# Optimization experiments

Measured on AMD Instinct MI355X. Metric: run time of the kernel, lower is better.

## Reference

```python
import jax, jax.numpy as jnp
import numpy as np

# Band partition of the 2049 frequency bins (BSRNN-style: narrow low bands, wide high bands)
_WIDTHS = [25] * 10 + [50] * 12 + [100] * 8 + [399]
_STARTS = np.concatenate([[0], np.cumsum(_WIDTHS)])
SUBBANDS = [(int(_STARTS[i]), int(_STARTS[i + 1])) for i in range(len(_WIDTHS))]
C_IN = 2          # stereo complex input channels
OUT_CH = 128      # band embedding dim
EPS = 1e-5        # GroupNorm eps
TOTAL_CH = sum(2 * C_IN * (e - s) for s, e in SUBBANDS)  # 8196


def setup_inputs() -> dict:
    key = jax.random.key(0)
    k1, k2, k3, k4 = jax.random.split(key, 4)
    B, F, T = 8, 2049, 512
    # x is view_as_real of a complex spectrogram: [B, C, F, T, 2]
    x = jax.random.normal(k1, (B, C_IN, F, T), dtype=jnp.float32)
    x = jnp.stack([x, jax.random.normal(k2, (B, C_IN, F, T), dtype=jnp.float32)], axis=-1)
    gamma = jax.random.uniform(k3, (TOTAL_CH,), dtype=jnp.float32)            # GroupNorm weight (concat over bands)
    beta = jax.random.normal(k4, (TOTAL_CH,), dtype=jnp.float32) * 0.1       # GroupNorm bias
    W = jax.random.normal(jax.random.fold_in(key, 5), (OUT_CH, TOTAL_CH), dtype=jnp.float32) * 0.02  # 1x1 conv weights, concat over bands
    b = jax.random.normal(jax.random.fold_in(key, 6), (len(SUBBANDS), OUT_CH), dtype=jnp.float32) * 0.02
    return {"x": x, "gamma": gamma, "beta": beta, "W": W, "b": b}


def reference(x, gamma, beta, W, b):
    # x: [B, C, F, T, 2] (real view of complex spectrogram)
    B, C, F, T, _ = x.shape
    outs = []
    off = 0
    for i, (s, e) in enumerate(SUBBANDS):
        ch = 2 * C * (e - s)
        # moveaxis(-1, 1): [B, 2, C, w, T] -> reshape [B, 2*C*w, T]
        h = jnp.moveaxis(x[:, :, s:e, :, :], -1, 1).reshape(B, ch, T)
        # GroupNorm(1, ch): normalize over (channel, time) per sample
        mu = jnp.mean(h, axis=(1, 2), keepdims=True)
        var = jnp.var(h, axis=(1, 2), keepdims=True)
        g = gamma[off:off + ch][None, :, None]
        bt = beta[off:off + ch][None, :, None]
        hn = (h - mu) * jax.lax.rsqrt(var + EPS) * g + bt
        # 1x1 Conv1d == per-timestep linear: [out, ch] x [B, ch, T] -> [B, out, T]
        y = jnp.einsum('oc,bct->bot', W[:, off:off + ch], hn) + b[i][None, :, None]
        outs.append(y)
        off += ch
    return jnp.stack(outs, axis=2)  # [B, OUT_CH, n_bands, T]
```

## Files before the change

kernel.cpp:

```cpp
#include <hip/hip_runtime.h>
#include <hip/hip_bf16.h>

typedef __attribute__((ext_vector_type(8))) short short8;
typedef __attribute__((ext_vector_type(4))) float f32x4;

#define NBANDS 31
#define BB 8
#define CCH 2
#define FF 2049
#define TTS 512
#define OUTC 128
#define TCH 8196
#define EPSV 1e-5f
#define NTILES 298

__constant__ int c_wid[NBANDS] = {
    25,25,25,25,25,25,25,25,25,25,
    50,50,50,50,50,50,50,50,50,50,50,50,
    100,100,100,100,100,100,100,100,
    399};
__constant__ int c_start[NBANDS] = {
    0,25,50,75,100,125,150,175,200,225,
    250,300,350,400,450,500,550,600,650,700,750,800,
    850,950,1050,1150,1250,1350,1450,1550,
    1650};
__constant__ int c_gb0[NBANDS + 1] = {
    0,2,4,6,8,10,12,14,16,18,
    20,24,28,32,36,40,44,48,52,56,60,64,
    68,75,82,89,96,103,110,117,
    124,149};
__constant__ int c_kpad[NBANDS] = {
    128,128,128,128,128,128,128,128,128,128,
    256,256,256,256,256,256,256,256,256,256,256,256,
    448,448,448,448,448,448,448,448,
    1600};
__constant__ int c_kbase[NBANDS] = {
    0,16384,32768,49152,65536,81920,98304,114688,131072,147456,
    163840,196608,229376,262144,294912,327680,360448,393216,425984,458752,491520,524288,
    557056,614400,671744,729088,786432,843776,901120,958464,
    1015808};
__constant__ int tb16b[NBANDS] = {
    0,4,8,12,16,20,24,28,32,36,
    40,48,56,64,72,80,88,96,104,112,120,128,
    136,150,164,178,192,206,220,234,
    248};
__constant__ int c_order[NBANDS] = {
    30,22,23,24,25,26,27,28,29,
    10,11,12,13,14,15,16,17,18,19,20,21,
    0,1,2,3,4,5,6,7,8,9};

#define NTRANS 2384
#define NWPREP 248
#define NWP2   992

__device__ inline unsigned short f2bf(float f) {
    __hip_bfloat16 h = __float2bfloat16(f);
    unsigned short u;
    __builtin_memcpy(&u, &h, 2);
    return u;
}

__device__ inline void gload_lds16(const void* g, void* l) {
    __builtin_amdgcn_global_load_lds((const __attribute__((address_space(1))) void*)g,
                                     (__attribute__((address_space(3))) void*)l, 16, 0, 0);
}

__global__ __launch_bounds__(256) void prep(const float* __restrict__ x,
                                            const float* __restrict__ W,
                                            const float* __restrict__ gamma,
                                            const float* __restrict__ beta,
                                            const float* __restrict__ bias,
                                            float* __restrict__ st,
                                            float* __restrict__ wgam,
                                            float* __restrict__ wcb,
                                            unsigned short* __restrict__ wgP,
                                            unsigned short* __restrict__ xb16) {
    __shared__ __align__(16) float ltf[16384];
    __shared__ float s1[256], s2[256];
    const int bid = blockIdx.x;
    const int tid = threadIdx.x;

    if (bid < NTRANS) {
        int g   = bid >> 4;
        int ycc = bid & 15;
        int band = 0;
        while (band + 1 < NBANDS && g >= c_gb0[band + 1]) band++;
        int fb = g - c_gb0[band];
        int b  = ycc >> 1;
        int cc = ycc & 1;
        int w = c_wid[band], s = c_start[band];
        int f0 = fb * 16;
        const float* xcc = x + (size_t)(b * CCH + cc) * FF * 1024;

#pragma unroll
        for (int r = 0; r < 16; ++r) {
            int row = s + min(f0 + r, w - 1);
            gload_lds16(xcc + (size_t)row * 1024 + tid * 4, &ltf[r * 1024 + tid * 4]);
        }
        __syncthreads();

        int taug = tb16b[band] + fb * 2 + cc;
        unsigned short* dst = xb16 + ((size_t)b * NTILES + taug) * 16384;
        float sum = 0.f, sq = 0.f;
#pragma unroll
        for (int it = 0; it < 8; ++it) {
            int idx = it * 256 + tid;
            int tb = idx >> 6, lane = idx & 63;
            int l15 = lane & 15, lg = lane >> 4;
            int t = tb * 16 + l15;
            short8 w8;
#pragma unroll
            for (int rr = 0; rr < 4; ++rr) {
                int floc = 4 * lg + rr;
                float2 v = *(const float2*)&ltf[floc * 1024 + t * 2];
                if (f0 + floc >= w) v = make_float2(0.f, 0.f);
                sum += v.x + v.y;
                sq  += v.x * v.x + v.y * v.y;
                w8[2 * rr]     = (short)f2bf(v.x);
                w8[2 * rr + 1] = (short)f2bf(v.y);
            }
            *(short8*)(dst + (size_t)idx * 8) = w8;
        }

        __syncthreads();
        s1[tid] = sum; s2[tid] = sq;
        __syncthreads();
        for (int st_ = 128; st_ > 0; st_ >>= 1) {
            if (tid < st_) { s1[tid] += s1[tid + st_]; s2[tid] += s2[tid + st_]; }
            __syncthreads();
        }
        if (tid == 0) {
            float* dp = st + (size_t)(g * 16 + ycc) * 2;
            dp[0] = s1[0];
            dp[1] = s2[0];
        }
    } else if (bid < NTRANS + NWPREP) {
        int r = bid - NTRANS;
        int band = r >> 3;
        int off = 4 * c_start[band];
        int ch  = 4 * c_wid[band];
        int o = (r & 7) * 16 + (tid >> 4);
        int lane = tid & 15;
        const float* wrow = W + (size_t)o * TCH + off;
        float sg = 0.f, sb = 0.f;
        for (int c = lane; c < ch; c += 16) {
            float wv = wrow[c];
            sg += wv * gamma[off + c];
            sb += wv * beta[off + c];
        }
        for (int m = 8; m; m >>= 1) {
            sg += __shfl_down(sg, m, 16);
            sb += __shfl_down(sb, m, 16);
        }
        if (lane == 0) {
            wgam[band * OUTC + o] = sg;
            wcb[band * OUTC + o]  = sb + bias[band * OUTC + o];
        }
    } else {
        int r = bid - (NTRANS + NWPREP);
        int band = r % NBANDS;
        int gy   = r / NBANDS;
        int w = c_wid[band];
        int s4 = 4 * c_start[band];
        int Kpad = c_kpad[band];
        int base = c_kbase[band];
        int N = OUTC * Kpad;
        for (int idx = gy * 256 + tid; idx < N; idx += 32 * 256) {
            int o = idx / Kpad;
            int k = idx - o * Kpad;
            int tau = k >> 5, fb = tau >> 1, cc = tau & 1;
            int fo = (k & 31) >> 1, ri = k & 1;
            int f = fb * 16 + fo;
            float val = 0.f;
            if (f < w) {
                int c = s4 + ri * 2 * w + cc * w + f;
                val = W[(size_t)o * TCH + c] * gamma[c];
            }
            int slot = (k >> 3) & 7;
            int pos = (k >> 6) * 8192 + o * 64 + ((slot ^ (o & 7)) * 8) + (k & 7);
            wgP[base + pos] = f2bf(val);
        }
    }
}

__global__ __launch_bounds__(256) void gemm_mfma(const unsigned short* __restrict__ xb16,
                                                 const unsigned short* __restrict__ wgP,
                                                 const float* __restrict__ st,
                                                 const float* __restrict__ wgam,
                                                 const float* __restrict__ wcb,
                                                 float* __restrict__ out) {
    const int band = c_order[blockIdx.y];
    const int b    = blockIdx.x >> 2;
    const int tti  = blockIdx.x & 3;
    const int tt0  = tti * 128;
    const int w    = c_wid[band];
    const int nch  = c_kpad[band] >> 6;
    const unsigned short* wgA = wgP + c_kbase[band];

    __shared__ unsigned short lA[2][8192];

    const int tid  = threadIdx.x;
    const int lane = tid & 63;
    const int wv   = tid >> 6;
    const int l15  = lane & 15;
    const int lg   = lane >> 4;

    const unsigned short* xbT = xb16 +
        (((size_t)b * NTILES + tb16b[band]) * 32 + tti * 8 + wv * 2) * 512 + lane * 8;

    f32x4 acc[8][2] = {};
    short8 bA[4], bB[4];

#define LOADB(c, dst) do {                                                     \
    _Pragma("unroll")                                                          \
    for (int kk = 0; kk < 2; ++kk)                                             \
        _Pragma("unroll")                                                      \
        for (int nf = 0; nf < 2; ++nf)                                         \
            dst[kk * 2 + nf] =                                                 \
                *(const short8*)(xbT + (size_t)((2 * (c) + kk) * 32 + nf) * 512); \
} while (0)

#define STAGE(c, buf) do {                                                     \
    const unsigned short* srcc = wgA + (size_t)(c) * 8192;                     \
    _Pragma("unroll")                                                          \
    for (int q = 0; q < 4; ++q)                                                \
        gload_lds16(srcc + q * 2048 + tid * 8, &lA[buf][q * 2048 + tid * 8]);  \
} while (0)

#define COMPUTE(br, buf) do {                                                  \
    _Pragma("unroll")                                                          \
    for (int kk = 0; kk < 2; ++kk) {                                           \
        short8 af[8];                                                          \
        _Pragma("unroll")                                                      \
        for (int m = 0; m < 8; ++m) {                                          \
            int o = m * 16 + l15;                                              \
            int slot = (lg + 4 * kk) ^ (o & 7);                                \
            af[m] = *(const short8*)&lA[buf][o * 64 + slot * 8];               \
        }                                                                      \
        _Pragma("unroll")                                                      \
        for (int nf = 0; nf < 2; ++nf)                                         \
            _Pragma("unroll")                                                  \
            for (int m = 0; m < 8; ++m)                                        \
                acc[m][nf] = __builtin_amdgcn_mfma_f32_16x16x32_bf16(          \
                    af[m], br[kk * 2 + nf], acc[m][nf], 0, 0, 0);              \
    }                                                                          \
} while (0)

    LOADB(0, bA);
    STAGE(0, 0);
    __syncthreads();
    for (int c = 0; c < nch; c += 2) {
        if (c + 1 < nch) { LOADB(c + 1, bB); STAGE(c + 1, 1); }
        COMPUTE(bA, 0);
        __syncthreads();
        if (c + 1 < nch) {
            if (c + 2 < nch) { LOADB(c + 2, bA); STAGE(c + 2, 0); }
            COMPUTE(bB, 1);
            __syncthreads();
        }
    }
#undef LOADB
#undef STAGE
#undef COMPUTE

    float sum = 0.f, sq = 0.f;
    {
        int g0 = c_gb0[band], g1 = c_gb0[band + 1];
        for (int g = g0; g < g1; ++g) {
            const float* p0 = st + (size_t)(g * 16 + b * 2) * 2;
            sum += p0[0] + p0[2];
            sq  += p0[1] + p0[3];
        }
    }
    const float Nf = (float)(w * 2048);
    const float mu = sum / Nf;
    const float rs = rsqrtf(sq / Nf - mu * mu + EPSV);

#pragma unroll
    for (int m = 0; m < 8; ++m) {
#pragma unroll
        for (int r = 0; r < 4; ++r) {
            int o = m * 16 + lg * 4 + r;
            float wg = wgam[band * OUTC + o];
            float cb = wcb[band * OUTC + o];
            size_t rowoff = (((size_t)b * OUTC + o) * NBANDS + band) * TTS;
#pragma unroll
            for (int nf = 0; nf < 2; ++nf) {
                int t = tt0 + wv * 32 + nf * 16 + l15;
                out[rowoff + t] = rs * (acc[m][nf][r] - mu * wg) + cb;
            }
        }
    }
}

extern "C" void kernel_launch(void* const* d_in, const int* in_sizes, int n_in,
                              void* d_out, int out_size, void* d_ws, size_t ws_size,
                              hipStream_t stream) {
    const float* x     = (const float*)d_in[0];
    const float* gamma = (const float*)d_in[1];
    const float* beta  = (const float*)d_in[2];
    const float* W     = (const float*)d_in[3];
    const float* bias  = (const float*)d_in[4];
    float* out = (float*)d_out;
    float* ws  = (float*)d_ws;

    float* st_part = ws;
    float* wgam    = ws + 5120;
    float* wcb     = ws + 9216;
    unsigned short* wgP  = (unsigned short*)(ws + 13312);
    unsigned short* xb16 = (unsigned short*)(ws + 640000);

    prep<<<NTRANS + NWPREP + NWP2, 256, 0, stream>>>(x, W, gamma, beta, bias,
                                                     st_part, wgam, wcb, wgP, xb16);
    gemm_mfma<<<dim3(32, NBANDS), 256, 0, stream>>>(xb16, wgP, st_part, wgam, wcb, out);
}
```

Measured before the change: 105.5 us.

## Split transpose blocks into four sub-blocks with smaller LDS and shuffle reductions

Each prep transpose block now handles 4 frequency rows instead of 16, so there are four times as many blocks and each uses a quarter of the LDS (16KB instead of 64KB). The goal is higher occupancy and better latency hiding in the memory-bound conversion pass. The tree reduction in shared memory is replaced by a wavefront shuffle reduction plus a 4-way sum. Partial stats become four times as numerous, so the workspace offsets move and the GEMM epilogue loops over more partials.

```diff
diff --git a/kernel.cpp b/kernel.cpp
--- a/kernel.cpp
+++ b/kernel.cpp
@@ -49,7 +49,7 @@
     10,11,12,13,14,15,16,17,18,19,20,21,
     0,1,2,3,4,5,6,7,8,9};
 
-#define NTRANS 2384
+#define NTRANS 9536
 #define NWPREP 248
 #define NWP2   992
 
@@ -75,25 +75,27 @@
                                             float* __restrict__ wcb,
                                             unsigned short* __restrict__ wgP,
                                             unsigned short* __restrict__ xb16) {
-    __shared__ __align__(16) float ltf[16384];
-    __shared__ float s1[256], s2[256];
+    __shared__ __align__(16) float ltf[4096];
+    __shared__ float s1[4], s2[4];
     const int bid = blockIdx.x;
     const int tid = threadIdx.x;
 
     if (bid < NTRANS) {
-        int g   = bid >> 4;
+        int g2  = bid >> 4;
         int ycc = bid & 15;
+        int g   = g2 >> 2;
+        int sub = g2 & 3;
         int band = 0;
         while (band + 1 < NBANDS && g >= c_gb0[band + 1]) band++;
         int fb = g - c_gb0[band];
         int b  = ycc >> 1;
         int cc = ycc & 1;
         int w = c_wid[band], s = c_start[band];
-        int f0 = fb * 16;
+        int f0 = fb * 16 + sub * 4;
         const float* xcc = x + (size_t)(b * CCH + cc) * FF * 1024;
 
 #pragma unroll
-        for (int r = 0; r < 16; ++r) {
+        for (int r = 0; r < 4; ++r) {
             int row = s + min(f0 + r, w - 1);
             gload_lds16(xcc + (size_t)row * 1024 + tid * 4, &ltf[r * 1024 + tid * 4]);
         }
@@ -103,36 +105,34 @@
         unsigned short* dst = xb16 + ((size_t)b * NTILES + taug) * 16384;
         float sum = 0.f, sq = 0.f;
 #pragma unroll
-        for (int it = 0; it < 8; ++it) {
-            int idx = it * 256 + tid;
-            int tb = idx >> 6, lane = idx & 63;
-            int l15 = lane & 15, lg = lane >> 4;
+        for (int i = 0; i < 2; ++i) {
+            int virt = i * 256 + tid;
+            int tb = virt >> 4, l15 = virt & 15;
             int t = tb * 16 + l15;
             short8 w8;
 #pragma unroll
             for (int rr = 0; rr < 4; ++rr) {
-                int floc = 4 * lg + rr;
-                float2 v = *(const float2*)&ltf[floc * 1024 + t * 2];
-                if (f0 + floc >= w) v = make_float2(0.f, 0.f);
+                float2 v = *(const float2*)&ltf[rr * 1024 + t * 2];
+                if (f0 + rr >= w) v = make_float2(0.f, 0.f);
                 sum += v.x + v.y;
                 sq  += v.x * v.x + v.y * v.y;
                 w8[2 * rr]     = (short)f2bf(v.x);
                 w8[2 * rr + 1] = (short)f2bf(v.y);
             }
-            *(short8*)(dst + (size_t)idx * 8) = w8;
-        }
-
+            *(short8*)(dst + ((size_t)tb * 64 + sub * 16 + l15) * 8) = w8;
+        }
+
+        for (int m = 32; m; m >>= 1) {
+            sum += __shfl_down(sum, m);
+            sq  += __shfl_down(sq, m);
+        }
+        int lane = tid & 63, wv = tid >> 6;
+        if (lane == 0) { s1[wv] = sum; s2[wv] = sq; }
         __syncthreads();
-        s1[tid] = sum; s2[tid] = sq;
-        __syncthreads();
-        for (int st_ = 128; st_ > 0; st_ >>= 1) {
-            if (tid < st_) { s1[tid] += s1[tid + st_]; s2[tid] += s2[tid + st_]; }
-            __syncthreads();
-        }
         if (tid == 0) {
-            float* dp = st + (size_t)(g * 16 + ycc) * 2;
-            dp[0] = s1[0];
-            dp[1] = s2[0];
+            float* dp = st + (size_t)(g2 * 16 + ycc) * 2;
+            dp[0] = s1[0] + s1[1] + s1[2] + s1[3];
+            dp[1] = s2[0] + s2[1] + s2[2] + s2[3];
         }
     } else if (bid < NTRANS + NWPREP) {
         int r = bid - NTRANS;
@@ -265,7 +265,7 @@
 
     float sum = 0.f, sq = 0.f;
     {
-        int g0 = c_gb0[band], g1 = c_gb0[band + 1];
+        int g0 = 4 * c_gb0[band], g1 = 4 * c_gb0[band + 1];
         for (int g = g0; g < g1; ++g) {
             const float* p0 = st + (size_t)(g * 16 + b * 2) * 2;
             sum += p0[0] + p0[2];
@@ -305,9 +305,9 @@
     float* ws  = (float*)d_ws;
 
     float* st_part = ws;
-    float* wgam    = ws + 5120;
-    float* wcb     = ws + 9216;
-    unsigned short* wgP  = (unsigned short*)(ws + 13312);
+    float* wgam    = ws + 19456;
+    float* wcb     = ws + 23552;
+    unsigned short* wgP  = (unsigned short*)(ws + 27648);
     unsigned short* xb16 = (unsigned short*)(ws + 640000);
 
     prep<<<NTRANS + NWPREP + NWP2, 256, 0, stream>>>(x, W, gamma, beta, bias,
```

New measurement: 121.3 us. 14.9% more time.
